# Performance work log

Measured on AMD Instinct MI355X. Metric: run time of the kernel, lower is better.

## Reference

```python
import jax, jax.numpy as jnp
import numpy as np

R = 2            # kernel_radius
N_IN = 64
N_OUT = 128
H, W = 209, 133  # input spatial dims (NHWC)
KH, KW = 4 * R + 1, 2 * R + 1


def hex_indices(radius):
    """Coordinates of hexagon cells inside a (4r+1, 2r+1) grid."""
    moves = np.array([[1, 1], [2, 0], [1, -1], [-1, -1], [-2, 0], [-1, 1]])
    out = [[2 * radius, radius]]
    for il in range(1, radius + 1):
        s = np.array([[2 * radius - 2 * il, radius]])
        cur = moves.repeat(il, axis=0).cumsum(axis=0)
        out.extend((s + cur).tolist())
    return np.array(out, dtype=np.int32)


def make_out_mask(h, w, r):
    out_h, out_w = h - 4 * r, w - 2 * r
    mr = (out_w - 1) // 2  # hex radius of the output mask
    f = np.zeros((mr * 4 + 1, mr * 2 + 1), dtype=np.float32)
    for ind in hex_indices(mr):
        f[tuple(ind)] = 1.0
    i_cut = (mr * 4 + 1 - out_h) // 2
    f = f[i_cut:-i_cut, :]
    return f.reshape(out_h, out_w, 1)


_HEX = hex_indices(R)               # [19, 2]
_N_IND = _HEX.shape[0]
# scatter indices matching MakeVariableIndices ordering:
# for ci in range(N_IN): for co in range(N_OUT): for j in range(n_ind)
_HW = np.tile(_HEX, (N_IN * N_OUT, 1))                       # [19*Nin*Nout, 2]
_CI = np.repeat(np.arange(N_IN), _N_IND * N_OUT)
_CO = np.tile(np.repeat(np.arange(N_OUT), _N_IND), N_IN)
_OUT_MASK = jnp.asarray(make_out_mask(H, W, R))              # [201, 129, 1]


def setup_inputs() -> dict:
    key = jax.random.key(0)
    k1, k2, k3 = jax.random.split(key, 3)
    # glorot-normal-ish scale for the sparse kernel weights
    fan = _N_IND * (N_IN + N_OUT) / 2.0
    sparse_weights = jax.random.normal(k1, (_N_IND * N_IN * N_OUT,), jnp.float32) * np.sqrt(1.0 / fan).astype(np.float32)
    x = jax.random.normal(k2, (16, H, W, N_IN), jnp.float32)
    offset = jax.random.normal(k3, (1, 1, 1, N_OUT), jnp.float32) * 0.1
    return {"x": x, "sparse_weights": sparse_weights, "offset": offset}


def reference(x, sparse_weights, offset):
    # rebuild dense hex-masked kernel [KH, KW, N_IN, N_OUT]
    kernel = jnp.zeros((KH, KW, N_IN, N_OUT), dtype=sparse_weights.dtype)
    kernel = kernel.at[_HW[:, 0], _HW[:, 1], _CI, _CO].set(sparse_weights)
    conv = jax.lax.conv_general_dilated(
        x, kernel, window_strides=(1, 1), padding="VALID",
        dimension_numbers=("NHWC", "HWIO", "NHWC"))
    return jax.nn.elu(conv + offset) * _OUT_MASK
```

## Files before the change

kernel.cpp:

```cpp
#include <hip/hip_runtime.h>
#include <math.h>

#define NB   16
#define HH   209
#define WW   133
#define CIN  64
#define COUT 128
#define OH   201
#define OW   129
#define NTAP 19
#define NW   (NTAP*CIN*COUT)

#define XS 72

typedef __attribute__((ext_vector_type(8))) __bf16 bf16x8;
typedef __attribute__((ext_vector_type(4))) float f32x4;
typedef __attribute__((ext_vector_type(4))) unsigned short us4;

__device__ __forceinline__ unsigned short f2bf(float f) {
  unsigned int u = __builtin_bit_cast(unsigned int, f);
  u += 0x7FFFu + ((u >> 16) & 1u);
  return (unsigned short)(u >> 16);
}

__global__ __launch_bounds__(256) void repack_w(const float* __restrict__ w,
                                                unsigned short* __restrict__ wt) {
  int gid = blockIdx.x * 256 + threadIdx.x;
  int ci = gid & 63;
  int co = (gid >> 6) & 127;
  int k  = gid >> 13;
  wt[gid] = f2bf(w[ci * (COUT * NTAP) + co * NTAP + k]);
}

__global__ __launch_bounds__(256) void conv_hex_mfma(const float* __restrict__ x,
                                                     const unsigned short* __restrict__ wt,
                                                     const float* __restrict__ offs,
                                                     float* __restrict__ out) {
  constexpr int c_start[9] = {0, 1, 3, 6, 8, 11, 13, 16, 18};
  constexpr int c_cnt[9]   = {1, 2, 3, 2, 3, 2, 3, 2, 1};
  constexpr int c_k[19]  = {18, 7,17, 6, 8,16, 1, 5, 0, 9,15, 2, 4, 3,10,14, 11,13, 12};
  constexpr int c_dw[19] = { 2, 3, 1, 2, 4, 0, 3, 1, 2, 4, 0, 3, 1, 2, 4, 0, 3, 1, 2};

  __shared__ unsigned short xs[2][82 * XS];

  const int tid  = threadIdx.x;
  const int lane = tid & 63;
  const int wv   = tid >> 6;
  const int l15  = lane & 15;
  const int quad = lane >> 4;
  const int n0   = wv * 32;

  const int bid = blockIdx.x;
  const int oi  = bid % OH;
  const int b   = bid / OH;
  const int par = oi & 1;
  const int na  = 65 - par;

  int ad = oi - 100; ad = ad < 0 ? -ad : ad;
  const int lim = 128 - ad;

  int a_lo_raw = 64 - lim - par;
  int a_lo = a_lo_raw <= 0 ? 0 : (a_lo_raw + 1) >> 1;
  int a_hi = (64 + lim - par) >> 1;
  if (a_hi > na - 1) a_hi = na - 1;

  const int f0 = a_lo >> 4;
  const int f1 = a_hi >> 4;
  const int nf = f1 - f0 + 1;
  const int p0 = f0 * 16;
  const int npos   = nf * 16;
  const int nchunk = (npos + 2) * 16;

  float* outb = out + (size_t)(b * OH + oi) * OW * COUT;

  {
    const float4 z = make_float4(0.f, 0.f, 0.f, 0.f);
    const int opar = par ^ 1;
    const int nopp = 65 - opar;
    for (int idx = tid; idx < nopp * 32; idx += 256) {
      int q  = idx >> 5;
      int c4 = idx & 31;
      *(float4*)(outb + (size_t)(opar + 2 * q) * COUT + c4 * 4) = z;
    }
    const int hi_start = p0 + npos;
    const int hi_cnt   = na > hi_start ? na - hi_start : 0;
    const int tot      = (p0 + hi_cnt) * 32;
    for (int idx = tid; idx < tot; idx += 256) {
      int q  = idx >> 5;
      int a  = q < p0 ? q : hi_start + (q - p0);
      int c4 = idx & 31;
      *(float4*)(outb + (size_t)(par + 2 * a) * COUT + c4 * 4) = z;
    }
  }

  f32x4 acc[5][2];
  #pragma unroll
  for (int i = 0; i < 5; ++i)
    #pragma unroll
    for (int j = 0; j < 2; ++j) acc[i][j] = (f32x4){0.f, 0.f, 0.f, 0.f};

  const float* xb = x + (size_t)b * (HH * WW * CIN);

  float4 stg[6];
  bf16x8 bfrag[3][2][2];

  auto load_stg = [&](int r) {
    const float* xr = xb + (size_t)(oi + r) * (WW * CIN);
    const int rpar = (par + r) & 1;
    #pragma unroll
    for (int i = 0; i < 6; ++i) {
      int c = tid + i * 256;
      if (c < nchunk) {
        int j  = c >> 4;
        int c4 = c & 15;
        int col = rpar + 2 * (p0 + j);
        if (col > WW - 1) col = WW - 1;
        stg[i] = *(const float4*)(xr + (size_t)col * CIN + c4 * 4);
      }
    }
  };
  auto store_stg = [&](int buf) {
    #pragma unroll
    for (int i = 0; i < 6; ++i) {
      int c = tid + i * 256;
      if (c < nchunk) {
        int j  = c >> 4;
        int c4 = c & 15;
        us4 o;
        o.x = f2bf(stg[i].x); o.y = f2bf(stg[i].y);
        o.z = f2bf(stg[i].z); o.w = f2bf(stg[i].w);
        *(us4*)(&xs[buf][j * XS + c4 * 4]) = o;
      }
    }
  };

  load_stg(0);
  store_stg(0);

  #pragma unroll
  for (int r = 0; r < 9; ++r) {
    {
      const int st = c_start[r], cnt = c_cnt[r];
      #pragma unroll
      for (int t = 0; t < 3; ++t) {
        if (t < cnt) {
          const unsigned short* wb = wt + (size_t)c_k[st + t] * (CIN * COUT);
          #pragma unroll
          for (int j = 0; j < 2; ++j) {
            const unsigned short* wn = wb + (size_t)(n0 + j * 16 + l15) * CIN + quad * 8;
            bfrag[t][0][j] = *(const bf16x8*)(wn);
            bfrag[t][1][j] = *(const bf16x8*)(wn + 32);
          }
        }
      }
    }
    if (r < 8) load_stg(r + 1);
    __syncthreads();

    {
      const int st = c_start[r], cnt = c_cnt[r];
      const unsigned short* bufp = xs[r & 1];
      #pragma unroll
      for (int t = 0; t < 3; ++t) {
        if (t < cnt) {
          const int s = (par + c_dw[st + t]) >> 1;
          #pragma unroll
          for (int ks = 0; ks < 2; ++ks) {
            #pragma unroll
            for (int mf = 0; mf < 5; ++mf) {
              if (mf < nf) {
                bf16x8 a = *(const bf16x8*)(&bufp[(mf * 16 + l15 + s) * XS + ks * 32 + quad * 8]);
                acc[mf][0] = __builtin_amdgcn_mfma_f32_16x16x32_bf16(a, bfrag[t][ks][0], acc[mf][0], 0, 0, 0);
                acc[mf][1] = __builtin_amdgcn_mfma_f32_16x16x32_bf16(a, bfrag[t][ks][1], acc[mf][1], 0, 0, 0);
              }
            }
          }
        }
      }
    }

    if (r < 8) store_stg((r + 1) & 1);
  }

  const float off0 = offs[n0 + l15];
  const float off1 = offs[n0 + 16 + l15];
  #pragma unroll
  for (int mf = 0; mf < 5; ++mf) {
    if (mf < nf) {
      #pragma unroll
      for (int r = 0; r < 4; ++r) {
        int a  = (f0 + mf) * 16 + quad * 4 + r;
        int oj = par + 2 * a;
        if (oj <= OW - 1) {
          int adj = oj - 64; adj = adj < 0 ? -adj : adj;
          bool valid = adj <= lim;
          float v0 = acc[mf][0][r] + off0;
          float v1 = acc[mf][1][r] + off1;
          float e0 = v0 > 0.f ? v0 : expm1f(v0);
          float e1 = v1 > 0.f ? v1 : expm1f(v1);
          outb[(size_t)oj * COUT + n0 + l15]      = valid ? e0 : 0.f;
          outb[(size_t)oj * COUT + n0 + 16 + l15] = valid ? e1 : 0.f;
        }
      }
    }
  }
}

extern "C" void kernel_launch(void* const* d_in, const int* in_sizes, int n_in,
                              void* d_out, int out_size, void* d_ws, size_t ws_size,
                              hipStream_t stream) {
  const float* x   = (const float*)d_in[0];
  const float* sw  = (const float*)d_in[1];
  const float* off = (const float*)d_in[2];
  float* out = (float*)d_out;

  unsigned short* wtb = (unsigned short*)d_ws;
  repack_w<<<NW / 256, 256, 0, stream>>>(sw, wtb);
  conv_hex_mfma<<<NB * OH, 256, 0, stream>>>(x, wtb, off, out);
}
```

Before: 414.9 us.

## Compute two output rows per block to reuse staged input rows and weights

Each block now computes a pair of adjacent output rows (even and odd parity) over a shared input window. Each staged input row feeds both rows, and weight fragments are ping-ponged between two register sets so one load serves row r for the first output and row r-1 for the second. This roughly halves global input traffic and the bf16 conversion work per output row. It also adds an XCD-aware block remap and launch_bounds(256,2), at the cost of doubled accumulator registers, a dynamic (not unrolled) row loop, and tap tables moved to constant memory.

```diff
diff --git a/kernel.cpp b/kernel.cpp
--- a/kernel.cpp
+++ b/kernel.cpp
@@ -10,12 +10,19 @@
 #define OW   129
 #define NTAP 19
 #define NW   (NTAP*CIN*COUT)
-
-#define XS 72
+#define XS   72
+#define MAXWIN 82
+#define NPAIR 101
+#define GRID (NB*NPAIR)
 
 typedef __attribute__((ext_vector_type(8))) __bf16 bf16x8;
 typedef __attribute__((ext_vector_type(4))) float f32x4;
 typedef __attribute__((ext_vector_type(4))) unsigned short us4;
+
+__constant__ int c_start[9] = {0, 1, 3, 6, 8, 11, 13, 16, 18};
+__constant__ int c_cnt[9]   = {1, 2, 3, 2, 3, 2, 3, 2, 1};
+__constant__ int c_k[19]  = {18, 7,17, 6, 8,16, 1, 5, 0, 9,15, 2, 4, 3,10,14, 11,13, 12};
+__constant__ int c_dw[19] = { 2, 3, 1, 2, 4, 0, 3, 1, 2, 4, 0, 3, 1, 2, 4, 0, 3, 1, 2};
 
 __device__ __forceinline__ unsigned short f2bf(float f) {
   unsigned int u = __builtin_bit_cast(unsigned int, f);
@@ -32,16 +39,11 @@
   wt[gid] = f2bf(w[ci * (COUT * NTAP) + co * NTAP + k]);
 }
 
-__global__ __launch_bounds__(256) void conv_hex_mfma(const float* __restrict__ x,
-                                                     const unsigned short* __restrict__ wt,
-                                                     const float* __restrict__ offs,
-                                                     float* __restrict__ out) {
-  constexpr int c_start[9] = {0, 1, 3, 6, 8, 11, 13, 16, 18};
-  constexpr int c_cnt[9]   = {1, 2, 3, 2, 3, 2, 3, 2, 1};
-  constexpr int c_k[19]  = {18, 7,17, 6, 8,16, 1, 5, 0, 9,15, 2, 4, 3,10,14, 11,13, 12};
-  constexpr int c_dw[19] = { 2, 3, 1, 2, 4, 0, 3, 1, 2, 4, 0, 3, 1, 2, 4, 0, 3, 1, 2};
-
-  __shared__ unsigned short xs[2][82 * XS];
+__global__ __launch_bounds__(256, 2) void conv_hex_mfma(const float* __restrict__ x,
+                                                        const unsigned short* __restrict__ wt,
+                                                        const float* __restrict__ offs,
+                                                        float* __restrict__ out) {
+  __shared__ unsigned short xs[2][MAXWIN * XS];
 
   const int tid  = threadIdx.x;
   const int lane = tid & 63;
@@ -51,69 +53,59 @@
   const int n0   = wv * 32;
 
   const int bid = blockIdx.x;
-  const int oi  = bid % OH;
-  const int b   = bid / OH;
-  const int par = oi & 1;
-  const int na  = 65 - par;
-
-  int ad = oi - 100; ad = ad < 0 ? -ad : ad;
-  const int lim = 128 - ad;
-
-  int a_lo_raw = 64 - lim - par;
-  int a_lo = a_lo_raw <= 0 ? 0 : (a_lo_raw + 1) >> 1;
-  int a_hi = (64 + lim - par) >> 1;
-  if (a_hi > na - 1) a_hi = na - 1;
-
-  const int f0 = a_lo >> 4;
-  const int f1 = a_hi >> 4;
-  const int nf = f1 - f0 + 1;
-  const int p0 = f0 * 16;
-  const int npos   = nf * 16;
-  const int nchunk = (npos + 2) * 16;
-
-  float* outb = out + (size_t)(b * OH + oi) * OW * COUT;
-
-  {
-    const float4 z = make_float4(0.f, 0.f, 0.f, 0.f);
-    const int opar = par ^ 1;
-    const int nopp = 65 - opar;
-    for (int idx = tid; idx < nopp * 32; idx += 256) {
-      int q  = idx >> 5;
-      int c4 = idx & 31;
-      *(float4*)(outb + (size_t)(opar + 2 * q) * COUT + c4 * 4) = z;
-    }
-    const int hi_start = p0 + npos;
-    const int hi_cnt   = na > hi_start ? na - hi_start : 0;
-    const int tot      = (p0 + hi_cnt) * 32;
-    for (int idx = tid; idx < tot; idx += 256) {
-      int q  = idx >> 5;
-      int a  = q < p0 ? q : hi_start + (q - p0);
-      int c4 = idx & 31;
-      *(float4*)(outb + (size_t)(par + 2 * a) * COUT + c4 * 4) = z;
-    }
+  const int wid = (bid & 7) * (GRID / 8) + (bid >> 3);
+  const int pair = wid % NPAIR;
+  const int b    = wid / NPAIR;
+  const int oi0  = pair * 2;
+  const bool has1 = pair < NPAIR - 1;
+
+  int ad0 = oi0 - 100; ad0 = ad0 < 0 ? -ad0 : ad0;
+  const int lim0 = 128 - ad0;
+  int al0 = 64 - lim0; al0 = al0 <= 0 ? 0 : (al0 + 1) >> 1;
+  int ah0 = (64 + lim0) >> 1; if (ah0 > 64) ah0 = 64;
+  const int f00 = al0 >> 4;
+  const int nf0 = (ah0 >> 4) - f00 + 1;
+  const int p00 = f00 * 16;
+
+  int lim1 = 0, f01 = 0, nf1 = 0, p01 = p00;
+  if (has1) {
+    int ad1 = oi0 + 1 - 100; ad1 = ad1 < 0 ? -ad1 : ad1;
+    lim1 = 128 - ad1;
+    int al1 = 63 - lim1; al1 = al1 <= 0 ? 0 : (al1 + 1) >> 1;
+    int ah1 = (63 + lim1) >> 1; if (ah1 > 63) ah1 = 63;
+    f01 = al1 >> 4; nf1 = (ah1 >> 4) - f01 + 1; p01 = f01 * 16;
   }
 
-  f32x4 acc[5][2];
+  const int W = p00 < p01 ? p00 : p01;
+  const int e0w = p00 + nf0 * 16, e1w = p01 + nf1 * 16;
+  const int endx = (e0w > e1w ? e0w : e1w) + 2;
+  const int nwin   = endx - W;
+  const int nchunk = nwin * 16;
+  const int R = has1 ? 10 : 9;
+
+  const float* xb = x + (size_t)b * (HH * WW * CIN);
+
+  f32x4 acc0[5][2], acc1[5][2];
   #pragma unroll
   for (int i = 0; i < 5; ++i)
     #pragma unroll
-    for (int j = 0; j < 2; ++j) acc[i][j] = (f32x4){0.f, 0.f, 0.f, 0.f};
-
-  const float* xb = x + (size_t)b * (HH * WW * CIN);
+    for (int j = 0; j < 2; ++j) {
+      acc0[i][j] = (f32x4){0.f, 0.f, 0.f, 0.f};
+      acc1[i][j] = (f32x4){0.f, 0.f, 0.f, 0.f};
+    }
 
   float4 stg[6];
-  bf16x8 bfrag[3][2][2];
+  bf16x8 bA[3][2][2], bB[3][2][2];
 
   auto load_stg = [&](int r) {
-    const float* xr = xb + (size_t)(oi + r) * (WW * CIN);
-    const int rpar = (par + r) & 1;
+    const float* xr = xb + (size_t)(oi0 + r) * (WW * CIN);
+    const int cp = r & 1;
     #pragma unroll
     for (int i = 0; i < 6; ++i) {
       int c = tid + i * 256;
       if (c < nchunk) {
-        int j  = c >> 4;
-        int c4 = c & 15;
-        int col = rpar + 2 * (p0 + j);
+        int m = c >> 4, c4 = c & 15;
+        int col = cp + 2 * (W + m);
         if (col > WW - 1) col = WW - 1;
         stg[i] = *(const float4*)(xr + (size_t)col * CIN + c4 * 4);
       }
@@ -124,86 +116,122 @@
     for (int i = 0; i < 6; ++i) {
       int c = tid + i * 256;
       if (c < nchunk) {
-        int j  = c >> 4;
-        int c4 = c & 15;
+        int m = c >> 4, c4 = c & 15;
         us4 o;
         o.x = f2bf(stg[i].x); o.y = f2bf(stg[i].y);
         o.z = f2bf(stg[i].z); o.w = f2bf(stg[i].w);
-        *(us4*)(&xs[buf][j * XS + c4 * 4]) = o;
-      }
-    }
-  };
-
+        *(us4*)(&xs[buf][m * XS + c4 * 4]) = o;
+      }
+    }
+  };
+  auto load_B = [&](bf16x8 (&bf)[3][2][2], int dh) {
+    const int st = c_start[dh], cnt = c_cnt[dh];
+    #pragma unroll
+    for (int t = 0; t < 3; ++t) {
+      if (t < cnt) {
+        const unsigned short* wb = wt + (size_t)c_k[st + t] * (CIN * COUT)
+                                      + (size_t)(n0 + l15) * CIN + quad * 8;
+        bf[t][0][0] = *(const bf16x8*)(wb);
+        bf[t][1][0] = *(const bf16x8*)(wb + 32);
+        bf[t][0][1] = *(const bf16x8*)(wb + 16 * CIN);
+        bf[t][1][1] = *(const bf16x8*)(wb + 16 * CIN + 32);
+      }
+    }
+  };
+  auto row_compute = [&](const unsigned short* bufp, const bf16x8 (&bf)[3][2][2],
+                         int dh, int p0g, int parg, int nfg, int r, f32x4 (&ag)[5][2]) {
+    const int st = c_start[dh], cnt = c_cnt[dh];
+    #pragma unroll
+    for (int t = 0; t < 3; ++t) {
+      if (t < cnt) {
+        const int dw = c_dw[st + t];
+        const int s  = p0g - W + ((parg + dw - (r & 1)) >> 1);
+        const unsigned short* ap = bufp + (s + l15) * XS + quad * 8;
+        #pragma unroll
+        for (int ks = 0; ks < 2; ++ks)
+          #pragma unroll
+          for (int mf = 0; mf < 5; ++mf)
+            if (mf < nfg) {
+              bf16x8 a = *(const bf16x8*)(ap + mf * 16 * XS + ks * 32);
+              ag[mf][0] = __builtin_amdgcn_mfma_f32_16x16x32_bf16(a, bf[t][ks][0], ag[mf][0], 0, 0, 0);
+              ag[mf][1] = __builtin_amdgcn_mfma_f32_16x16x32_bf16(a, bf[t][ks][1], ag[mf][1], 0, 0, 0);
+            }
+      }
+    }
+  };
+
+  load_B(bA, 0);
   load_stg(0);
   store_stg(0);
 
-  #pragma unroll
-  for (int r = 0; r < 9; ++r) {
+  #pragma unroll 1
+  for (int r = 0; r < 10; r += 2) {
     {
-      const int st = c_start[r], cnt = c_cnt[r];
-      #pragma unroll
-      for (int t = 0; t < 3; ++t) {
-        if (t < cnt) {
-          const unsigned short* wb = wt + (size_t)c_k[st + t] * (CIN * COUT);
-          #pragma unroll
-          for (int j = 0; j < 2; ++j) {
-            const unsigned short* wn = wb + (size_t)(n0 + j * 16 + l15) * CIN + quad * 8;
-            bfrag[t][0][j] = *(const bf16x8*)(wn);
-            bfrag[t][1][j] = *(const bf16x8*)(wn + 32);
+      __syncthreads();
+      const unsigned short* bufp = xs[0];
+      if (r + 1 < R) load_stg(r + 1);
+      if (has1 && r >= 1) row_compute(bufp, bB, r - 1, p01, 1, nf1, r, acc1);
+      if (r + 1 <= 8) load_B(bB, r + 1);
+      row_compute(bufp, bA, r, p00, 0, nf0, r, acc0);
+      if (r + 1 < R) store_stg(1);
+    }
+    const int ro = r + 1;
+    if (ro < R) {
+      __syncthreads();
+      const unsigned short* bufp = xs[1];
+      if (ro + 1 < R) load_stg(ro + 1);
+      if (has1) row_compute(bufp, bA, ro - 1, p01, 1, nf1, ro, acc1);
+      if (ro + 1 <= 8) load_B(bA, ro + 1);
+      if (ro <= 8) row_compute(bufp, bB, ro, p00, 0, nf0, ro, acc0);
+      if (ro + 1 < R) store_stg(0);
+    }
+  }
+
+  auto finish_row = [&](int oi_g, int parg, int limg, int f0g, int nfg, f32x4 (&ag)[5][2]) {
+    float* outb = out + (size_t)(b * OH + oi_g) * OW * COUT;
+    const float4 z = make_float4(0.f, 0.f, 0.f, 0.f);
+    const int opar = parg ^ 1;
+    const int nopp = 65 - opar;
+    for (int idx = tid; idx < nopp * 32; idx += 256) {
+      int q = idx >> 5, c4 = idx & 31;
+      *(float4*)(outb + (size_t)(opar + 2 * q) * COUT + c4 * 4) = z;
+    }
+    const int nag = 65 - parg;
+    const int p0g = f0g * 16;
+    const int hi  = p0g + nfg * 16;
+    const int hic = nag > hi ? nag - hi : 0;
+    const int tot = (p0g + hic) * 32;
+    for (int idx = tid; idx < tot; idx += 256) {
+      int q = idx >> 5, c4 = idx & 31;
+      int a = q < p0g ? q : hi + (q - p0g);
+      *(float4*)(outb + (size_t)(parg + 2 * a) * COUT + c4 * 4) = z;
+    }
+    const float off0 = offs[n0 + l15];
+    const float off1 = offs[n0 + 16 + l15];
+    #pragma unroll
+    for (int mf = 0; mf < 5; ++mf) {
+      if (mf < nfg) {
+        #pragma unroll
+        for (int rr = 0; rr < 4; ++rr) {
+          int a  = (f0g + mf) * 16 + quad * 4 + rr;
+          int oj = parg + 2 * a;
+          if (oj <= OW - 1) {
+            int adj = oj - 64; adj = adj < 0 ? -adj : adj;
+            bool valid = adj <= limg;
+            float v0 = ag[mf][0][rr] + off0;
+            float v1 = ag[mf][1][rr] + off1;
+            float e0v = v0 > 0.f ? v0 : expm1f(v0);
+            float e1v = v1 > 0.f ? v1 : expm1f(v1);
+            outb[(size_t)oj * COUT + n0 + l15]      = valid ? e0v : 0.f;
+            outb[(size_t)oj * COUT + n0 + 16 + l15] = valid ? e1v : 0.f;
           }
         }
       }
     }
-    if (r < 8) load_stg(r + 1);
-    __syncthreads();
-
-    {
-      const int st = c_start[r], cnt = c_cnt[r];
-      const unsigned short* bufp = xs[r & 1];
-      #pragma unroll
-      for (int t = 0; t < 3; ++t) {
-        if (t < cnt) {
-          const int s = (par + c_dw[st + t]) >> 1;
-          #pragma unroll
-          for (int ks = 0; ks < 2; ++ks) {
-            #pragma unroll
-            for (int mf = 0; mf < 5; ++mf) {
-              if (mf < nf) {
-                bf16x8 a = *(const bf16x8*)(&bufp[(mf * 16 + l15 + s) * XS + ks * 32 + quad * 8]);
-                acc[mf][0] = __builtin_amdgcn_mfma_f32_16x16x32_bf16(a, bfrag[t][ks][0], acc[mf][0], 0, 0, 0);
-                acc[mf][1] = __builtin_amdgcn_mfma_f32_16x16x32_bf16(a, bfrag[t][ks][1], acc[mf][1], 0, 0, 0);
-              }
-            }
-          }
-        }
-      }
-    }
-
-    if (r < 8) store_stg((r + 1) & 1);
-  }
-
-  const float off0 = offs[n0 + l15];
-  const float off1 = offs[n0 + 16 + l15];
-  #pragma unroll
-  for (int mf = 0; mf < 5; ++mf) {
-    if (mf < nf) {
-      #pragma unroll
-      for (int r = 0; r < 4; ++r) {
-        int a  = (f0 + mf) * 16 + quad * 4 + r;
-        int oj = par + 2 * a;
-        if (oj <= OW - 1) {
-          int adj = oj - 64; adj = adj < 0 ? -adj : adj;
-          bool valid = adj <= lim;
-          float v0 = acc[mf][0][r] + off0;
-          float v1 = acc[mf][1][r] + off1;
-          float e0 = v0 > 0.f ? v0 : expm1f(v0);
-          float e1 = v1 > 0.f ? v1 : expm1f(v1);
-          outb[(size_t)oj * COUT + n0 + l15]      = valid ? e0 : 0.f;
-          outb[(size_t)oj * COUT + n0 + 16 + l15] = valid ? e1 : 0.f;
-        }
-      }
-    }
-  }
+  };
+
+  finish_row(oi0, 0, lim0, f00, nf0, acc0);
+  if (has1) finish_row(oi0 + 1, 1, lim1, f01, nf1, acc1);
 }
 
 extern "C" void kernel_launch(void* const* d_in, const int* in_sizes, int n_in,
@@ -216,5 +244,5 @@
 
   unsigned short* wtb = (unsigned short*)d_ws;
   repack_w<<<NW / 256, 256, 0, stream>>>(sw, wtb);
-  conv_hex_mfma<<<NB * OH, 256, 0, stream>>>(x, wtb, off, out);
-}
+  conv_hex_mfma<<<GRID, 256, 0, stream>>>(x, wtb, off, out);
+}
```

After: 448.6 us. +8.1%, slower.
